# Kernel optimization log

Hardware: AMD Instinct MI355X
Metric: run time of the kernel (lower is better)

## Reference

```python
import jax, jax.numpy as jnp
import numpy as np

EMB = 1024
HEADS = 16
HEAD_DIM = EMB // HEADS


def setup_inputs() -> dict:
    key = jax.random.key(0)
    ks = jax.random.split(key, 9)
    s = 1.0 / np.sqrt(EMB)
    x = jax.random.normal(ks[0], (4, 2048, EMB), dtype=jnp.float32)
    Wq = jax.random.uniform(ks[1], (EMB, EMB), minval=-s, maxval=s, dtype=jnp.float32)
    bq = jax.random.uniform(ks[2], (EMB,), minval=-s, maxval=s, dtype=jnp.float32)
    Wk = jax.random.uniform(ks[3], (EMB, EMB), minval=-s, maxval=s, dtype=jnp.float32)
    bk = jax.random.uniform(ks[4], (EMB,), minval=-s, maxval=s, dtype=jnp.float32)
    Wv = jax.random.uniform(ks[5], (EMB, EMB), minval=-s, maxval=s, dtype=jnp.float32)
    bv = jax.random.uniform(ks[6], (EMB,), minval=-s, maxval=s, dtype=jnp.float32)
    Wo = jax.random.uniform(ks[7], (EMB, EMB), minval=-s, maxval=s, dtype=jnp.float32)
    bo = jax.random.uniform(ks[8], (EMB,), minval=-s, maxval=s, dtype=jnp.float32)
    return {"x": x, "Wq": Wq, "bq": bq, "Wk": Wk, "bk": bk, "Wv": Wv, "bv": bv, "Wo": Wo, "bo": bo}


def reference(x, Wq, bq, Wk, bk, Wv, bv, Wo, bo):
    B, S, E = x.shape
    # QKV projections (torch Linear: y = x W^T + b)
    q = x @ Wq.T + bq
    k = x @ Wk.T + bk
    v = x @ Wv.T + bv
    # split heads -> [B, H, S, Dh]
    q = q.reshape(B, S, HEADS, HEAD_DIM).transpose(0, 2, 1, 3)
    k = k.reshape(B, S, HEADS, HEAD_DIM).transpose(0, 2, 1, 3)
    v = v.reshape(B, S, HEADS, HEAD_DIM).transpose(0, 2, 1, 3)
    # NOTE: module scales by 1/sqrt(emb_size), NOT 1/sqrt(head_dim)
    scale = 1.0 / jnp.sqrt(jnp.asarray(E, dtype=x.dtype))
    energy = jnp.einsum('bhqd,bhkd->bhqk', q, k) * scale
    attention = jax.nn.softmax(energy, axis=-1)
    out = jnp.einsum('bhqk,bhkd->bhqd', attention, v)
    out = out.transpose(0, 2, 1, 3).reshape(B, S, E)
    return out @ Wo.T + bo
```

## Files before the change

### kernel.cpp

```cpp
#include <hip/hip_runtime.h>


typedef __bf16 bf16;
typedef __attribute__((ext_vector_type(4))) short shortx4;
typedef __attribute__((ext_vector_type(8))) short short8;
typedef __attribute__((ext_vector_type(4))) float floatx4;
typedef __attribute__((ext_vector_type(2))) unsigned int uintx2;
typedef __attribute__((ext_vector_type(4))) unsigned int uintx4;

#define MFMA16(a, b, c) __builtin_amdgcn_mfma_f32_16x16x32_bf16((a), (b), (c), 0, 0, 0)

#define LDS_STRIDE 56

__device__ __forceinline__ float fast_exp2(float x) {
    float r;
    asm("v_exp_f32 %0, %1" : "=v"(r) : "v"(x));
    return r;
}
__device__ __forceinline__ unsigned int cvt_pk_bf16(float lo, float hi) {
    unsigned int r;
    asm("v_cvt_pk_bf16_f32 %0, %1, %2" : "=v"(r) : "v"(lo), "v"(hi));
    return r;
}

__device__ __forceinline__ void async16(const bf16* __restrict__ g, short* l) {
    __builtin_amdgcn_global_load_lds((const __attribute__((address_space(1))) void*)g,
                                     (__attribute__((address_space(3))) void*)l, 16, 0, 0);
}

__device__ __forceinline__ short8 frag8(const bf16* __restrict__ p) {
    return *(const short8*)p;
}
__device__ __forceinline__ short8 frag8(const float* __restrict__ p) {
    const floatx4 a = *(const floatx4*)p;
    const floatx4 b = *(const floatx4*)(p + 4);
    short8 r;
#pragma unroll
    for (int j = 0; j < 4; j++) {
        r[j]     = __builtin_bit_cast(short, (bf16)a[j]);
        r[4 + j] = __builtin_bit_cast(short, (bf16)b[j]);
    }
    return r;
}

__global__ __launch_bounds__(256) void to_bf16(
    const float* __restrict__ in, bf16* __restrict__ out, int n8)
{
    const int i = blockIdx.x * 256 + threadIdx.x;
    if (i >= n8) return;
    const floatx4 a = *(const floatx4*)(in + (size_t)i * 8);
    const floatx4 b = *(const floatx4*)(in + (size_t)i * 8 + 4);
    short8 r;
#pragma unroll
    for (int j = 0; j < 4; j++) {
        r[j]     = __builtin_bit_cast(short, (bf16)a[j]);
        r[4 + j] = __builtin_bit_cast(short, (bf16)b[j]);
    }
    *(short8*)((short*)out + (size_t)i * 8) = r;
}

__global__ __launch_bounds__(256) void to_bf16_w4(
    const float* __restrict__ Wq, const float* __restrict__ Wk,
    const float* __restrict__ Wv, const float* __restrict__ Wo,
    bf16* __restrict__ out)
{
    const int i = blockIdx.x * 256 + threadIdx.x;
    const int t = i >> 17;
    const int j = i & 131071;
    const float* src = (t == 0) ? Wq : (t == 1) ? Wk : (t == 2) ? Wv : Wo;
    const floatx4 a = *(const floatx4*)(src + (size_t)j * 8);
    const floatx4 b = *(const floatx4*)(src + (size_t)j * 8 + 4);
    short8 r;
#pragma unroll
    for (int jj = 0; jj < 4; jj++) {
        r[jj]     = __builtin_bit_cast(short, (bf16)a[jj]);
        r[4 + jj] = __builtin_bit_cast(short, (bf16)b[jj]);
    }
    *(short8*)((short*)out + (size_t)t * 1048576 + (size_t)j * 8) = r;
}

__device__ __forceinline__ void gemm128_p3(
    const bf16* __restrict__ A, const bf16* __restrict__ B,
    int m0, int n0, short* As, short* Bs, floatx4 acc[4][4])
{
    const int tid  = threadIdx.x;
    const int lane = tid & 63;
    const int w    = tid >> 6;
    const int wu   = __builtin_amdgcn_readfirstlane(w);
    const int wm   = w >> 1, wn = w & 1;
    const int g    = lane >> 4, c = lane & 15;
    const int ar   = lane >> 2;
    const int aq   = ((lane & 3) ^ (ar & 3)) * 8;
    const int aswz = (g ^ (c & 3)) * 8;

#pragma unroll
    for (int mi = 0; mi < 4; mi++)
#pragma unroll
        for (int ni = 0; ni < 4; ni++)
            acc[mi][ni] = (floatx4){0.f, 0.f, 0.f, 0.f};

    const bf16* Arow0 = A + (size_t)(m0 + w * 32 + ar) * 1024 + aq;
    const bf16* Arow1 = A + (size_t)(m0 + w * 32 + 16 + ar) * 1024 + aq;
    const bf16* Brow0 = B + (size_t)(n0 + w * 32 + ar) * 1024 + aq;
    const bf16* Brow1 = B + (size_t)(n0 + w * 32 + 16 + ar) * 1024 + aq;

    {
        short* Ad = As + wu * 1024;
        short* Bd = Bs + wu * 1024;
        async16(Arow0, Ad);        async16(Arow1, Ad + 512);
        async16(Brow0, Bd);        async16(Brow1, Bd + 512);
        async16(Arow0 + 32, Ad + 4096);  async16(Arow1 + 32, Ad + 4096 + 512);
        async16(Brow0 + 32, Bd + 4096);  async16(Brow1 + 32, Bd + 4096 + 512);
    }

    int cur = 0;
    for (int t = 0; t < 32; ++t) {
        if (t < 31) asm volatile("s_waitcnt vmcnt(4)" ::: "memory");
        else        asm volatile("s_waitcnt vmcnt(0)" ::: "memory");
        __builtin_amdgcn_sched_barrier(0);
        __builtin_amdgcn_s_barrier();
        __builtin_amdgcn_sched_barrier(0);

        const short* Ac = As + cur * 4096;
        const short* Bc = Bs + cur * 4096;
        short8 af[4], bfr[4];
#pragma unroll
        for (int mi = 0; mi < 4; mi++)
            af[mi] = *(const short8*)(Ac + (wm * 64 + mi * 16 + c) * 32 + aswz);
#pragma unroll
        for (int ni = 0; ni < 4; ni++)
            bfr[ni] = *(const short8*)(Bc + (wn * 64 + ni * 16 + c) * 32 + aswz);
#pragma unroll
        for (int mi = 0; mi < 4; mi++)
#pragma unroll
            for (int ni = 0; ni < 4; ni++)
                acc[mi][ni] = MFMA16(af[mi], bfr[ni], acc[mi][ni]);

        if (t < 30) {
            const int kn  = (t + 2) * 32;
            const int nb  = (cur == 0) ? 2 : cur - 1;
            short* Ad = As + nb * 4096 + wu * 1024;
            short* Bd = Bs + nb * 4096 + wu * 1024;
            async16(Arow0 + kn, Ad);   async16(Arow1 + kn, Ad + 512);
            async16(Brow0 + kn, Bd);   async16(Brow1 + kn, Bd + 512);
        }
        cur = (cur == 2) ? 0 : cur + 1;
    }
}

__device__ __forceinline__ void gemm128_fallback(
    const bf16* __restrict__ A, const float* __restrict__ B,
    int m0, int n0, short* As, short* Bs, floatx4 acc[4][4])
{
    const int tid  = threadIdx.x;
    const int lane = tid & 63;
    const int w    = tid >> 6;
    const int wu   = __builtin_amdgcn_readfirstlane(w);
    const int wm   = w >> 1, wn = w & 1;
    const int g    = lane >> 4, c = lane & 15;
    const int ar = lane >> 2;
    const int aq = ((lane & 3) ^ (ar & 3)) * 8;
    const int lrow = tid >> 2;
    const int lc8  = (tid & 3) * 8;

#pragma unroll
    for (int mi = 0; mi < 4; mi++)
#pragma unroll
        for (int ni = 0; ni < 4; ni++)
            acc[mi][ni] = (floatx4){0.f, 0.f, 0.f, 0.f};

    const int aswz = (g ^ (c & 3)) * 8;

    for (int k0 = 0; k0 < 1024; k0 += 32) {
        async16(A + (size_t)(m0 + w * 32 + ar) * 1024 + k0 + aq,      As + wu * 1024);
        async16(A + (size_t)(m0 + w * 32 + 16 + ar) * 1024 + k0 + aq, As + wu * 1024 + 512);
        *(short8*)(Bs + lrow * LDS_STRIDE + lc8) =
            frag8(B + (size_t)(n0 + lrow) * 1024 + k0 + lc8);
        *(short8*)(Bs + (lrow + 64) * LDS_STRIDE + lc8) =
            frag8(B + (size_t)(n0 + lrow + 64) * 1024 + k0 + lc8);
        __syncthreads();

        short8 af[4], bfr[4];
#pragma unroll
        for (int mi = 0; mi < 4; mi++)
            af[mi] = *(const short8*)(As + (wm * 64 + mi * 16 + c) * 32 + aswz);
#pragma unroll
        for (int ni = 0; ni < 4; ni++)
            bfr[ni] = *(const short8*)(Bs + (wn * 64 + ni * 16 + c) * LDS_STRIDE + g * 8);
#pragma unroll
        for (int mi = 0; mi < 4; mi++)
#pragma unroll
            for (int ni = 0; ni < 4; ni++)
                acc[mi][ni] = MFMA16(af[mi], bfr[ni], acc[mi][ni]);
        __syncthreads();
    }
}

template <typename TB>
__global__ __launch_bounds__(256) void qkv_gemm(
    const bf16* __restrict__ Xb,
    const TB* __restrict__ Wq, const TB* __restrict__ Wk, const TB* __restrict__ Wv,
    const float* __restrict__ bq, const float* __restrict__ bk, const float* __restrict__ bv,
    bf16* __restrict__ qkv)
{
    __shared__ __align__(16) short As[(sizeof(TB) == 2) ? 12288 : 4096];
    __shared__ __align__(16) short Bs[(sizeof(TB) == 2) ? 12288 : 128 * LDS_STRIDE];

    const int lin = (blockIdx.z * 64 + blockIdx.y) * 8 + blockIdx.x;
    const int xcd = lin & 7;
    const int i   = lin >> 3;
    const int z   = i >> 6;
    const int m0  = (xcd * 8 + ((i >> 3) & 7)) * 128;
    const int n0  = (i & 7) * 128;

    const TB* W       = (z == 0) ? Wq : (z == 1) ? Wk : Wv;
    const float* bias = (z == 0) ? bq : (z == 1) ? bk : bv;
    bf16* outz = qkv + (size_t)z * (8192u * 1024u);

    floatx4 acc[4][4];
    if constexpr (sizeof(TB) == 2)
        gemm128_p3(Xb, (const bf16*)W, m0, n0, As, Bs, acc);
    else
        gemm128_fallback(Xb, (const float*)W, m0, n0, As, Bs, acc);

    const int lane = threadIdx.x & 63;
    const int w = threadIdx.x >> 6;
    const int wm = w >> 1, wn = w & 1;
    const int g = lane >> 4, c = lane & 15;

    if (z == 2) {
#pragma unroll
        for (int ni = 0; ni < 4; ni++) {
            const int n = n0 + wn * 64 + ni * 16 + c;
            const float bb = bias[n];
            const int h = n >> 6, d = n & 63;
#pragma unroll
            for (int mi = 0; mi < 4; mi++) {
                const int m = m0 + wm * 64 + mi * 16 + g * 4;
                const int b = m >> 11, s = m & 2047;
                shortx4 st;
#pragma unroll
                for (int r = 0; r < 4; r++)
                    st[r] = __builtin_bit_cast(short, (bf16)(acc[mi][ni][r] + bb));
                *(shortx4*)&outz[(((size_t)((b << 4) | h)) * 64 + d) * 2048 + s] = st;
            }
        }
    } else {
#pragma unroll
        for (int ni = 0; ni < 4; ni++) {
            const int n = n0 + wn * 64 + ni * 16 + c;
            const float bb = bias[n];
            const int h = n >> 6, d = n & 63;
#pragma unroll
            for (int mi = 0; mi < 4; mi++) {
#pragma unroll
                for (int r = 0; r < 4; r++) {
                    const int m = m0 + wm * 64 + mi * 16 + g * 4 + r;
                    const int b = m >> 11, s = m & 2047;
                    outz[(((size_t)((b << 4) | h)) * 2048 + s) * 64 + d] =
                        (bf16)(acc[mi][ni][r] + bb);
                }
            }
        }
    }
}

__global__ __launch_bounds__(512, 2) void attn_kernel(
    const bf16* __restrict__ qkv, bf16* __restrict__ attn_out)
{
    __shared__ __align__(16) short Ks[2][128 * 64];
    __shared__ __align__(16) short Vs[2][64 * 128];

    const int lin  = blockIdx.y * gridDim.x + blockIdx.x;
    const int slot = lin >> 3;
    const int bh   = (lin & 7) * 8 + (slot >> 3);
    const int q0   = (slot & 7) * 256;

    const size_t HSTRIDE = 2048u * 64u;
    const bf16* __restrict__ Q  = qkv + (size_t)bh * HSTRIDE;
    const bf16* __restrict__ Kp = qkv + 8192u * 1024u + (size_t)bh * HSTRIDE;
    const bf16* __restrict__ Vt = qkv + 2u * 8192u * 1024u + (size_t)bh * HSTRIDE;

    const int tid  = threadIdx.x;
    const int lane = tid & 63;
    const int w    = tid >> 6;
    const int wu   = __builtin_amdgcn_readfirstlane(w);
    const int g    = lane >> 4, c = lane & 15;

    const float C2 = 0.04508422002778f;

    const int krow_off = lane >> 3;
    const int kchunk   = (lane & 7) ^ (lane >> 3);
    const int vrow_off = lane >> 4;
    const int vchunk   = (lane & 15) ^ ((w * 4 + (lane >> 4)) & 15);

    short8 qf[2][2];
#pragma unroll
    for (int qb = 0; qb < 2; qb++)
#pragma unroll
        for (int ks = 0; ks < 2; ks++)
            qf[qb][ks] = *(const short8*)(Q + (size_t)(q0 + w * 32 + qb * 16 + c) * 64
                                            + ks * 32 + g * 8);

    floatx4 o[2][4];
#pragma unroll
    for (int mi = 0; mi < 2; mi++)
#pragma unroll
        for (int di = 0; di < 4; di++)
            o[mi][di] = (floatx4){0.f, 0.f, 0.f, 0.f};
    float l_run[2] = {0.f, 0.f};

#pragma unroll
    for (int s = 0; s < 2; s++) {
        const int row = s * 64 + w * 8 + krow_off;
        async16(Kp + (size_t)row * 64 + kchunk * 8, &Ks[0][(s * 64 + wu * 8) * 64]);
    }
#pragma unroll
    for (int s = 0; s < 2; s++) {
        const int row = s * 32 + w * 4 + vrow_off;
        async16(Vt + (size_t)row * 2048 + vchunk * 8, &Vs[0][(s * 32 + wu * 4) * 128]);
    }
    __syncthreads();

    int cur = 0;
    for (int kb = 0; kb < 16; kb++) {
        if (kb < 15) {
            const int kn = (kb + 1) * 128;
#pragma unroll
            for (int s = 0; s < 2; s++) {
                const int row = s * 64 + w * 8 + krow_off;
                async16(Kp + (size_t)(kn + row) * 64 + kchunk * 8,
                        &Ks[cur ^ 1][(s * 64 + wu * 8) * 64]);
            }
#pragma unroll
            for (int s = 0; s < 2; s++) {
                const int row = s * 32 + w * 4 + vrow_off;
                async16(Vt + (size_t)row * 2048 + kn + vchunk * 8,
                        &Vs[cur ^ 1][(s * 32 + wu * 4) * 128]);
            }
        }

        const short* __restrict__ Kc = &Ks[cur][0];
        const short* __restrict__ Vc = &Vs[cur][0];

        floatx4 sAcc[2][8];
#pragma unroll
        for (int qb = 0; qb < 2; qb++)
#pragma unroll
            for (int ni = 0; ni < 8; ni++)
                sAcc[qb][ni] = (floatx4){0.f, 0.f, 0.f, 0.f};
#pragma unroll
        for (int ks = 0; ks < 2; ks++)
#pragma unroll
            for (int ni = 0; ni < 8; ni++) {
                const short8 kf = *(const short8*)(
                    Kc + (16 * ni + c) * 64 + (((ks * 4 + g) ^ (c & 7)) * 8));
                sAcc[0][ni] = MFMA16(kf, qf[0][ks], sAcc[0][ni]);
                sAcc[1][ni] = MFMA16(kf, qf[1][ks], sAcc[1][ni]);
            }

        unsigned int lo[2][8], hi[2][8];
#pragma unroll
        for (int qb = 0; qb < 2; qb++) {
            floatx4 sv = {0.f, 0.f, 0.f, 0.f};
#pragma unroll
            for (int ni = 0; ni < 8; ni++) {
#pragma unroll
                for (int r = 0; r < 4; r++) {
                    const float p = fast_exp2(sAcc[qb][ni][r] * C2);
                    sAcc[qb][ni][r] = p;
                    sv[r] += p;
                }
                lo[qb][ni] = cvt_pk_bf16(sAcc[qb][ni][0], sAcc[qb][ni][1]);
                hi[qb][ni] = cvt_pk_bf16(sAcc[qb][ni][2], sAcc[qb][ni][3]);
            }
            float sum = (sv[0] + sv[1]) + (sv[2] + sv[3]);
            sum += __shfl_xor(sum, 16);
            sum += __shfl_xor(sum, 32);
            l_run[qb] += sum;
        }

#pragma unroll
        for (int t = 0; t < 4; t++) {
            const short8 pf0 = __builtin_bit_cast(short8,
                (uintx4){lo[0][2 * t], hi[0][2 * t], lo[0][2 * t + 1], hi[0][2 * t + 1]});
            const short8 pf1 = __builtin_bit_cast(short8,
                (uintx4){lo[1][2 * t], hi[1][2 * t], lo[1][2 * t + 1], hi[1][2 * t + 1]});
#pragma unroll
            for (int di = 0; di < 4; di++) {
                const int rowb = (16 * di + c) * 128 + 4 * (g & 1);
                const uintx2 vlo = *(const uintx2*)(
                    Vc + rowb + (((4 * t + (g >> 1)) ^ c) * 8));
                const uintx2 vhi = *(const uintx2*)(
                    Vc + rowb + (((4 * t + 2 + (g >> 1)) ^ c) * 8));
                const short8 vf = __builtin_bit_cast(short8,
                    (uintx4){vlo[0], vlo[1], vhi[0], vhi[1]});
                o[0][di] = MFMA16(pf0, vf, o[0][di]);
                o[1][di] = MFMA16(pf1, vf, o[1][di]);
            }
        }

        if (kb < 15) __syncthreads();
        cur ^= 1;
    }

    const int b = bh >> 4, h = bh & 15;
#pragma unroll
    for (int mi = 0; mi < 2; mi++) {
#pragma unroll
        for (int r = 0; r < 4; r++) {
            const int src = (lane & 48) | (g * 4 + r);
            const float linv = 1.0f / __shfl(l_run[mi], src);
            const int srow = q0 + w * 32 + mi * 16 + g * 4 + r;
#pragma unroll
            for (int di = 0; di < 4; di++) {
                attn_out[((size_t)(b * 2048 + srow)) * 1024 + h * 64 + di * 16 + c] =
                    (bf16)(o[mi][di][r] * linv);
            }
        }
    }
}

template <typename TB>
__global__ __launch_bounds__(256) void out_gemm(
    const bf16* __restrict__ A, const TB* __restrict__ Wo,
    const float* __restrict__ bo, float* __restrict__ C)
{
    __shared__ __align__(16) short As[(sizeof(TB) == 2) ? 12288 : 4096];
    __shared__ __align__(16) short Bs[(sizeof(TB) == 2) ? 12288 : 128 * LDS_STRIDE];

    const int lin = blockIdx.y * 8 + blockIdx.x;
    const int xcd = lin & 7;
    const int i   = lin >> 3;
    const int m0  = (xcd * 8 + (i >> 3)) * 128;
    const int n0  = (i & 7) * 128;

    floatx4 acc[4][4];
    if constexpr (sizeof(TB) == 2)
        gemm128_p3(A, (const bf16*)Wo, m0, n0, As, Bs, acc);
    else
        gemm128_fallback(A, (const float*)Wo, m0, n0, As, Bs, acc);

    const int lane = threadIdx.x & 63;
    const int w = threadIdx.x >> 6;
    const int wm = w >> 1, wn = w & 1;
    const int g = lane >> 4, c = lane & 15;

#pragma unroll
    for (int ni = 0; ni < 4; ni++) {
        const int n = n0 + wn * 64 + ni * 16 + c;
        const float bb = bo[n];
#pragma unroll
        for (int mi = 0; mi < 4; mi++) {
#pragma unroll
            for (int r = 0; r < 4; r++) {
                const int m = m0 + wm * 64 + mi * 16 + g * 4 + r;
                C[(size_t)m * 1024 + n] = acc[mi][ni][r] + bb;
            }
        }
    }
}

extern "C" void kernel_launch(void* const* d_in, const int* in_sizes, int n_in,
                              void* d_out, int out_size, void* d_ws, size_t ws_size,
                              hipStream_t stream)
{
    const float* x  = (const float*)d_in[0];
    const float* Wq = (const float*)d_in[1];
    const float* bq = (const float*)d_in[2];
    const float* Wk = (const float*)d_in[3];
    const float* bk = (const float*)d_in[4];
    const float* Wv = (const float*)d_in[5];
    const float* bv = (const float*)d_in[6];
    const float* Wo = (const float*)d_in[7];
    const float* bo = (const float*)d_in[8];
    float* out = (float*)d_out;

    bf16* qkv  = (bf16*)d_ws;
    bf16* attn = qkv + 3u * 8192u * 1024u;
    bf16* xb   = attn;

    const size_t base = 64u * 1024u * 1024u;
    const bool haveW = ws_size >= base + 8u * 1024u * 1024u;
    bf16* wb = (bf16*)((char*)d_ws + base);

    to_bf16<<<dim3(4096), dim3(256), 0, stream>>>(x, xb, 1048576);

    if (haveW) {
        to_bf16_w4<<<dim3(2048), dim3(256), 0, stream>>>(Wq, Wk, Wv, Wo, wb);
        qkv_gemm<bf16><<<dim3(8, 64, 3), dim3(256), 0, stream>>>(
            xb, wb, wb + 1048576u, wb + 2u * 1048576u, bq, bk, bv, qkv);
    } else {
        qkv_gemm<float><<<dim3(8, 64, 3), dim3(256), 0, stream>>>(
            xb, Wq, Wk, Wv, bq, bk, bv, qkv);
    }

    attn_kernel<<<dim3(8, 64), dim3(512), 0, stream>>>(qkv, attn);

    if (haveW) {
        out_gemm<bf16><<<dim3(8, 64), dim3(256), 0, stream>>>(
            attn, wb + 3u * 1048576u, bo, out);
    } else {
        out_gemm<float><<<dim3(8, 64), dim3(256), 0, stream>>>(attn, Wo, bo, out);
    }
}
```

Before: 278.4 us.

## Single-buffer V tile with split waitcnt barriers to fit three blocks per CU

Drops the V double buffer so each block uses 48KB of LDS instead of 64KB. The launch bound rises to 3 blocks of 512 threads, which targets higher occupancy. V for the current key block is now issued at the start of each iteration and waited on with explicit vmcnt counts just before the PV MFMAs, so the load overlaps the QK^T and softmax work. The cost is an extra barrier per iteration and exposed V latency, and the higher occupancy target may cap registers and cause spills.

```diff
diff --git a/kernel.cpp b/kernel.cpp
--- a/kernel.cpp
+++ b/kernel.cpp
@@ -265,11 +265,11 @@
     }
 }
 
-__global__ __launch_bounds__(512, 2) void attn_kernel(
+__global__ __launch_bounds__(512, 3) void attn_kernel(
     const bf16* __restrict__ qkv, bf16* __restrict__ attn_out)
 {
     __shared__ __align__(16) short Ks[2][128 * 64];
-    __shared__ __align__(16) short Vs[2][64 * 128];
+    __shared__ __align__(16) short Vs[64 * 128];
 
     const int lin  = blockIdx.y * gridDim.x + blockIdx.x;
     const int slot = lin >> 3;
@@ -315,15 +315,17 @@
         const int row = s * 64 + w * 8 + krow_off;
         async16(Kp + (size_t)row * 64 + kchunk * 8, &Ks[0][(s * 64 + wu * 8) * 64]);
     }
-#pragma unroll
-    for (int s = 0; s < 2; s++) {
-        const int row = s * 32 + w * 4 + vrow_off;
-        async16(Vt + (size_t)row * 2048 + vchunk * 8, &Vs[0][(s * 32 + wu * 4) * 128]);
-    }
-    __syncthreads();
 
     int cur = 0;
     for (int kb = 0; kb < 16; kb++) {
+        const int k0 = kb * 128;
+
+#pragma unroll
+        for (int s = 0; s < 2; s++) {
+            const int row = s * 32 + w * 4 + vrow_off;
+            async16(Vt + (size_t)row * 2048 + k0 + vchunk * 8,
+                    &Vs[(s * 32 + wu * 4) * 128]);
+        }
         if (kb < 15) {
             const int kn = (kb + 1) * 128;
 #pragma unroll
@@ -332,16 +334,15 @@
                 async16(Kp + (size_t)(kn + row) * 64 + kchunk * 8,
                         &Ks[cur ^ 1][(s * 64 + wu * 8) * 64]);
             }
-#pragma unroll
-            for (int s = 0; s < 2; s++) {
-                const int row = s * 32 + w * 4 + vrow_off;
-                async16(Vt + (size_t)row * 2048 + kn + vchunk * 8,
-                        &Vs[cur ^ 1][(s * 32 + wu * 4) * 128]);
-            }
-        }
+        }
+
+        if (kb < 15) asm volatile("s_waitcnt vmcnt(4)" ::: "memory");
+        else         asm volatile("s_waitcnt vmcnt(2)" ::: "memory");
+        __builtin_amdgcn_sched_barrier(0);
+        __builtin_amdgcn_s_barrier();
+        __builtin_amdgcn_sched_barrier(0);
 
         const short* __restrict__ Kc = &Ks[cur][0];
-        const short* __restrict__ Vc = &Vs[cur][0];
 
         floatx4 sAcc[2][8];
 #pragma unroll
@@ -380,6 +381,12 @@
             l_run[qb] += sum;
         }
 
+        if (kb < 15) asm volatile("s_waitcnt vmcnt(2)" ::: "memory");
+        else         asm volatile("s_waitcnt vmcnt(0)" ::: "memory");
+        __builtin_amdgcn_sched_barrier(0);
+        __builtin_amdgcn_s_barrier();
+        __builtin_amdgcn_sched_barrier(0);
+
 #pragma unroll
         for (int t = 0; t < 4; t++) {
             const short8 pf0 = __builtin_bit_cast(short8,
@@ -390,9 +397,9 @@
             for (int di = 0; di < 4; di++) {
                 const int rowb = (16 * di + c) * 128 + 4 * (g & 1);
                 const uintx2 vlo = *(const uintx2*)(
-                    Vc + rowb + (((4 * t + (g >> 1)) ^ c) * 8));
+                    Vs + rowb + (((4 * t + (g >> 1)) ^ c) * 8));
                 const uintx2 vhi = *(const uintx2*)(
-                    Vc + rowb + (((4 * t + 2 + (g >> 1)) ^ c) * 8));
+                    Vs + rowb + (((4 * t + 2 + (g >> 1)) ^ c) * 8));
                 const short8 vf = __builtin_bit_cast(short8,
                     (uintx4){vlo[0], vlo[1], vhi[0], vhi[1]});
                 o[0][di] = MFMA16(pf0, vf, o[0][di]);
@@ -400,7 +407,10 @@
             }
         }
 
-        if (kb < 15) __syncthreads();
+        if (kb < 15) {
+            __builtin_amdgcn_s_barrier();
+            __builtin_amdgcn_sched_barrier(0);
+        }
         cur ^= 1;
     }
 
```

Result: slower. 326.5 us (+17.3%).
